# Optimization experiments

Hardware: AMD Instinct MI355X
Metric: run time of the kernel (lower is better)

The kernel has to match this reference:

```python
import jax, jax.numpy as jnp
import numpy as np

NUM_HEADS = 16
NEG_INF = -1e18


def setup_inputs() -> dict:
    key = jax.random.key(0)
    ks = jax.random.split(key, 9)
    T, B, D = 2048, 2, 1024
    s = 1.0 / np.sqrt(D)
    return {
        "query": jax.random.normal(ks[0], (T, B, D), jnp.float32),
        "q_w": jax.random.normal(ks[1], (D, D), jnp.float32) * s,
        "q_b": jax.random.normal(ks[2], (D,), jnp.float32) * 0.02,
        "k_w": jax.random.normal(ks[3], (D, D), jnp.float32) * s,
        "k_b": jax.random.normal(ks[4], (D,), jnp.float32) * 0.02,
        "v_w": jax.random.normal(ks[5], (D, D), jnp.float32) * s,
        "v_b": jax.random.normal(ks[6], (D,), jnp.float32) * 0.02,
        "out_w": jax.random.normal(ks[7], (D, D), jnp.float32) * s,
        "out_b": jax.random.normal(ks[8], (D,), jnp.float32) * 0.02,
    }


def reference(query, q_w, q_b, k_w, k_b, v_w, v_b, out_w, out_b):
    # query: [T, B, D] (Time x Batch x Channel). Self-attention, causal mask,
    # dropout=0, need_weights=True.
    T, B, D = query.shape
    H = NUM_HEADS
    hd = D // H
    scaling = 1.0 / jnp.sqrt(jnp.asarray(hd, query.dtype))

    q = (query @ q_w.T + q_b) * scaling
    k = query @ k_w.T + k_b
    v = query @ v_w.T + v_b

    def split_heads(x):  # [T, B, D] -> [B, H, T, hd]
        return x.reshape(T, B, H, hd).transpose(1, 2, 0, 3)

    qh, kh, vh = split_heads(q), split_heads(k), split_heads(v)

    # scores: [B, H, T, T]
    scores = jnp.einsum("bhtd,bhsd->bhts", qh, kh)
    causal = jnp.triu(jnp.full((T, T), NEG_INF, dtype=scores.dtype), k=1)
    scores = scores + causal

    probs = jax.nn.softmax(scores, axis=-1)
    attn = jnp.einsum("bhts,bhsd->bhtd", probs, vh)  # [B, H, T, hd]
    attn = attn.transpose(2, 0, 1, 3).reshape(T, B, D)
    out = attn @ out_w.T + out_b

    # averaged attention weights over heads: [B, T, T]
    avg_weights = probs.sum(axis=1) / H
    return out, avg_weights
```

## Files before the change

kernel.cpp:

```cpp
#include <hip/hip_runtime.h>
#include <hip/hip_bf16.h>
#include <stdint.h>

typedef __hip_bfloat16 bf16;
using short8 = __attribute__((ext_vector_type(8))) short;
using f32x4  = __attribute__((ext_vector_type(4))) float;

#define TDIM 2048
#define BDIM 2
#define DDIM 1024
#define HNUM 16
#define HD   64
#define MDIM 4096
#define M0   16.0f
#define L2E  1.44269504088896f
#define M0B  23.0831207f

__device__ __forceinline__ f32x4 mfma16(short8 a, short8 b, f32x4 c) {
  return __builtin_amdgcn_mfma_f32_16x16x32_bf16(a, b, c, 0, 0, 0);
}

__device__ __forceinline__ float fexp2(float s) {
  return __builtin_amdgcn_exp2f(__builtin_fmaf(s, L2E, -M0B));
}

union S8 { short8 v; bf16 h[8]; };
union P4 { uint2 u; bf16 h[4]; };

__global__ __launch_bounds__(256) void cast_all_kernel(
    const float* __restrict__ q, const float* __restrict__ wq,
    const float* __restrict__ wk, const float* __restrict__ wv,
    const float* __restrict__ wo, bf16* __restrict__ dst) {
  int t4 = blockIdx.x * blockDim.x + threadIdx.x;
  int idx = t4 * 4;
  const float* s;
  if (idx < 4194304)      s = q  + idx;
  else if (idx < 5242880) s = wq + (idx - 4194304);
  else if (idx < 6291456) s = wk + (idx - 5242880);
  else if (idx < 7340032) s = wv + (idx - 6291456);
  else                    s = wo + (idx - 7340032);
  float4 v = *(const float4*)s;
  union { ushort4 u; bf16 b[4]; } pk;
  pk.b[0] = __float2bfloat16(v.x);
  pk.b[1] = __float2bfloat16(v.y);
  pk.b[2] = __float2bfloat16(v.z);
  pk.b[3] = __float2bfloat16(v.w);
  *(ushort4*)(dst + idx) = pk.u;
}

__global__ __launch_bounds__(256, 2) void qkv_kernel(
    const bf16* __restrict__ X, const bf16* __restrict__ Wq,
    const bf16* __restrict__ Wk, const bf16* __restrict__ Wv,
    const float* __restrict__ qb, const float* __restrict__ kb,
    const float* __restrict__ vb, bf16* __restrict__ Qo,
    bf16* __restrict__ Ko, bf16* __restrict__ Vto) {
  __shared__ __align__(16) bf16 Xs[128][72];
  __shared__ __align__(16) bf16 Qs[64][72];
  __shared__ __align__(16) bf16 Ks[64][72];
  __shared__ __align__(16) bf16 Vs[64][72];
  const int tid  = threadIdx.x;
  const int lane = tid & 63, wave = tid >> 6;
  const int m0 = blockIdx.y * 128, n0 = blockIdx.x * 64;
  const int wm = (wave >> 1) * 64, wn = (wave & 1) * 32;
  const int fr = lane & 15, quad = lane >> 4, q8 = quad * 8;
  const int r = tid >> 3, cc = (tid & 7) * 8;
  f32x4 aq[4][2] = {}, ak[4][2] = {}, av[2][4] = {};
  const bf16* xp = X  + (size_t)(m0 + r) * DDIM + cc;
  const bf16* qp = Wq + (size_t)(n0 + r) * DDIM + cc;
  const bf16* kp = Wk + (size_t)(n0 + r) * DDIM + cc;
  const bf16* vp = Wv + (size_t)(n0 + r) * DDIM + cc;
  uint4 xv0, xv1, xv2, xv3, qv0, qv1, kv0, kv1, vv0, vv1;
#define QKV_LD(K0)                                                  \
  do {                                                              \
    xv0 = *(const uint4*)(xp + (K0));                               \
    xv1 = *(const uint4*)(xp + (size_t)32 * DDIM + (K0));           \
    xv2 = *(const uint4*)(xp + (size_t)64 * DDIM + (K0));           \
    xv3 = *(const uint4*)(xp + (size_t)96 * DDIM + (K0));           \
    qv0 = *(const uint4*)(qp + (K0));                               \
    qv1 = *(const uint4*)(qp + (size_t)32 * DDIM + (K0));           \
    kv0 = *(const uint4*)(kp + (K0));                               \
    kv1 = *(const uint4*)(kp + (size_t)32 * DDIM + (K0));           \
    vv0 = *(const uint4*)(vp + (K0));                               \
    vv1 = *(const uint4*)(vp + (size_t)32 * DDIM + (K0));           \
  } while (0)
  QKV_LD(0);
  for (int k0 = 0; k0 < DDIM; k0 += 64) {
    __syncthreads();
    *(uint4*)&Xs[r][cc]      = xv0;
    *(uint4*)&Xs[r + 32][cc] = xv1;
    *(uint4*)&Xs[r + 64][cc] = xv2;
    *(uint4*)&Xs[r + 96][cc] = xv3;
    *(uint4*)&Qs[r][cc]      = qv0;
    *(uint4*)&Qs[r + 32][cc] = qv1;
    *(uint4*)&Ks[r][cc]      = kv0;
    *(uint4*)&Ks[r + 32][cc] = kv1;
    *(uint4*)&Vs[r][cc]      = vv0;
    *(uint4*)&Vs[r + 32][cc] = vv1;
    __syncthreads();
    if (k0 + 64 < DDIM) QKV_LD(k0 + 64);
#pragma unroll
    for (int kk = 0; kk < 2; kk++) {
      const int ko = kk * 32 + q8;
      short8 xf[4], qf[2], kf[2], vf[2];
#pragma unroll
      for (int i = 0; i < 4; i++)
        xf[i] = *(const short8*)&Xs[wm + i * 16 + fr][ko];
#pragma unroll
      for (int j = 0; j < 2; j++) {
        qf[j] = *(const short8*)&Qs[wn + j * 16 + fr][ko];
        kf[j] = *(const short8*)&Ks[wn + j * 16 + fr][ko];
        vf[j] = *(const short8*)&Vs[wn + j * 16 + fr][ko];
      }
#pragma unroll
      for (int i = 0; i < 4; i++)
#pragma unroll
        for (int j = 0; j < 2; j++) {
          aq[i][j] = mfma16(xf[i], qf[j], aq[i][j]);
          ak[i][j] = mfma16(xf[i], kf[j], ak[i][j]);
          av[j][i] = mfma16(vf[j], xf[i], av[j][i]);
        }
    }
  }
#undef QKV_LD
#pragma unroll
  for (int mt = 0; mt < 4; mt++)
#pragma unroll
    for (int nt = 0; nt < 2; nt++)
#pragma unroll
      for (int i = 0; i < 4; i++) {
        int gm = m0 + wm + mt * 16 + quad * 4 + i;
        int gn = n0 + wn + nt * 16 + fr;
        int t = gm >> 1, bb = gm & 1, h = gn >> 6, e = gn & 63;
        size_t o = ((size_t)(bb * HNUM + h) * TDIM + t) * HD + e;
        Qo[o] = __float2bfloat16((aq[mt][nt][i] + qb[gn]) * 0.125f);
        Ko[o] = __float2bfloat16(ak[mt][nt][i] + kb[gn]);
      }
#pragma unroll
  for (int vt = 0; vt < 2; vt++)
#pragma unroll
    for (int xt = 0; xt < 4; xt++)
#pragma unroll
      for (int i = 0; i < 4; i++) {
        int gf = n0 + wn + vt * 16 + quad * 4 + i;
        int gt = m0 + wm + xt * 16 + fr;
        int t = gt >> 1, bb = gt & 1, h = gf >> 6, e = gf & 63;
        Vto[((size_t)(bb * HNUM + h) * HD + e) * TDIM + t] =
            __float2bfloat16(av[vt][xt][i] + vb[gf]);
      }
}

__global__ __launch_bounds__(256) void gemm_out_kernel(
    const bf16* __restrict__ P0, const bf16* __restrict__ P1,
    const bf16* __restrict__ Bw, const float* __restrict__ l0buf,
    const float* __restrict__ l1buf, const float* __restrict__ bias,
    float* __restrict__ of32) {
  __shared__ __align__(16) bf16 As[64][72];
  __shared__ __align__(16) bf16 Bs[64][72];
  __shared__ float sInv[64][16];
  const int tid  = threadIdx.x;
  const int lane = tid & 63, wave = tid >> 6;
  const int m0 = blockIdx.y * 64, n0 = blockIdx.x * 64;
  const int wm = (wave >> 1) * 32, wn = (wave & 1) * 32;
  const int fr = lane & 15, quad = lane >> 4, q8 = quad * 8;
  const int ldr = tid >> 3, ldc = (tid & 7) * 8;
#pragma unroll
  for (int e = 0; e < 4; e++) {
    int idx = tid * 4 + e;
    int row = idx >> 4, h = idx & 15;
    int gm = m0 + row, t = gm >> 1, bb = gm & 1;
    size_t li = (size_t)(bb * HNUM + h) * TDIM + t;
    sInv[row][h] = 1.0f / (l0buf[li] + l1buf[li]);
  }
  f32x4 acc[2][2] = {};
  const size_t ar0 = (size_t)(m0 + ldr) * DDIM + ldc;
  const size_t ar1 = ar0 + (size_t)32 * DDIM;
  const bf16* bp0 = Bw + (size_t)(n0 + ldr) * DDIM + ldc;
  const bf16* bp1 = bp0 + (size_t)32 * DDIM;
  short8 p00v, p10v, p01v, p11v;
  uint4 bv0, bv1;
#define OUT_LD(K0)                                  \
  do {                                              \
    p00v = *(const short8*)&P0[ar0 + (K0)];         \
    p10v = *(const short8*)&P1[ar0 + (K0)];         \
    p01v = *(const short8*)&P0[ar1 + (K0)];         \
    p11v = *(const short8*)&P1[ar1 + (K0)];         \
    bv0  = *(const uint4*)(bp0 + (K0));             \
    bv1  = *(const uint4*)(bp1 + (K0));             \
  } while (0)
  OUT_LD(0);
  __syncthreads();
  for (int k0 = 0; k0 < DDIM; k0 += 64) {
    const float inv0 = sInv[ldr][k0 >> 6];
    const float inv1 = sInv[ldr + 32][k0 >> 6];
    S8 s00, s10, s01, s11, w0, w1;
    s00.v = p00v; s10.v = p10v; s01.v = p01v; s11.v = p11v;
#pragma unroll
    for (int k = 0; k < 8; k++) {
      w0.h[k] = __float2bfloat16(
          (__bfloat162float(s00.h[k]) + __bfloat162float(s10.h[k])) * inv0);
      w1.h[k] = __float2bfloat16(
          (__bfloat162float(s01.h[k]) + __bfloat162float(s11.h[k])) * inv1);
    }
    __syncthreads();
    *(short8*)&As[ldr][ldc]      = w0.v;
    *(short8*)&As[ldr + 32][ldc] = w1.v;
    *(uint4*)&Bs[ldr][ldc]       = bv0;
    *(uint4*)&Bs[ldr + 32][ldc]  = bv1;
    __syncthreads();
    if (k0 + 64 < DDIM) OUT_LD(k0 + 64);
#pragma unroll
    for (int kk = 0; kk < 2; kk++) {
      const int ko = kk * 32 + q8;
      short8 af0, af1, bf0, bf1;
      af0 = *(const short8*)&As[wm + fr][ko];
      af1 = *(const short8*)&As[wm + 16 + fr][ko];
      bf0 = *(const short8*)&Bs[wn + fr][ko];
      bf1 = *(const short8*)&Bs[wn + 16 + fr][ko];
      acc[0][0] = mfma16(af0, bf0, acc[0][0]);
      acc[0][1] = mfma16(af0, bf1, acc[0][1]);
      acc[1][0] = mfma16(af1, bf0, acc[1][0]);
      acc[1][1] = mfma16(af1, bf1, acc[1][1]);
    }
  }
#undef OUT_LD
#pragma unroll
  for (int mt = 0; mt < 2; mt++)
#pragma unroll
    for (int nt = 0; nt < 2; nt++)
#pragma unroll
      for (int i = 0; i < 4; i++) {
        int gm = m0 + wm + mt * 16 + quad * 4 + i;
        int gn = n0 + wn + nt * 16 + fr;
        of32[(size_t)gm * DDIM + gn] = acc[mt][nt][i] + bias[gn];
      }
}

__global__ __launch_bounds__(256) void attn_split_kernel(
    const bf16* __restrict__ Q, const bf16* __restrict__ K,
    const bf16* __restrict__ Vt, bf16* __restrict__ P0o,
    bf16* __restrict__ P1o, float* __restrict__ l0buf,
    float* __restrict__ l1buf) {
  __shared__ __align__(16) bf16 Ks[2][64][40];
  __shared__ __align__(16) bf16 Vs[2][64][40];
  __shared__ __align__(16) bf16 pt[4][32][72];
  const int tid = threadIdx.x, lane = tid & 63, wave = tid >> 6;
  const int bid = blockIdx.x;
  const int part = bid & 1, bh = (bid >> 1) & 31, t128 = 15 - (bid >> 6);
  const int b = bh >> 4, h = bh & 15;
  const int t0 = t128 * 128 + wave * 32;
  const int fr = lane & 15, quad = lane >> 4, q8 = quad * 8;
  const bf16* Qp = Q + ((size_t)bh * TDIM + t0) * HD;
  const bf16* Kp = K + (size_t)bh * TDIM * HD;
  const bf16* Vp = Vt + (size_t)bh * HD * TDIM;
  short8 aq[2][2];
  aq[0][0] = *(const short8*)&Qp[fr * HD + q8];
  aq[0][1] = *(const short8*)&Qp[fr * HD + 32 + q8];
  aq[1][0] = *(const short8*)&Qp[(16 + fr) * HD + q8];
  aq[1][1] = *(const short8*)&Qp[(16 + fr) * HD + 32 + q8];
  const int Cb = 2 * t128 + 2, C0 = t128 + 1;
  const int clo = part ? C0 : 0, chi = part ? Cb : C0;
  const int sr0 = tid >> 3, scc = (tid & 7) * 8, sr1 = sr0 + 32;
  const int ssub = scc >> 5, scol = scc & 31;
  f32x4 oacc[2][4] = {};
  float lsum[2] = {0.f, 0.f};
  uint4 kv0, kv1, vv0, vv1;
  auto ldglob = [&](int c) {
    int s0 = c * 64;
    kv0 = *(const uint4*)&Kp[(size_t)(s0 + sr0) * HD + scc];
    kv1 = *(const uint4*)&Kp[(size_t)(s0 + sr1) * HD + scc];
    vv0 = *(const uint4*)&Vp[(size_t)sr0 * TDIM + s0 + scc];
    vv1 = *(const uint4*)&Vp[(size_t)sr1 * TDIM + s0 + scc];
  };
  ldglob(clo);
  for (int c = clo; c < chi; c++) {
    __syncthreads();
    *(uint4*)&Ks[ssub][sr0][scol] = kv0;
    *(uint4*)&Ks[ssub][sr1][scol] = kv1;
    *(uint4*)&Vs[ssub][sr0][scol] = vv0;
    *(uint4*)&Vs[ssub][sr1][scol] = vv1;
    __syncthreads();
    if (c + 1 < chi) ldglob(c + 1);
    const int s0 = c * 64;
    if (s0 > t0 + 31) continue;
    f32x4 scT[2][4] = {};
#pragma unroll
    for (int j = 0; j < 4; j++) {
      short8 k0f = *(const short8*)&Ks[0][j * 16 + fr][q8];
      short8 k1f = *(const short8*)&Ks[1][j * 16 + fr][q8];
      scT[0][j] = mfma16(k0f, aq[0][0], scT[0][j]);
      scT[0][j] = mfma16(k1f, aq[0][1], scT[0][j]);
      scT[1][j] = mfma16(k0f, aq[1][0], scT[1][j]);
      scT[1][j] = mfma16(k1f, aq[1][1], scT[1][j]);
    }
#pragma unroll
    for (int g = 0; g < 2; g++) {
      const int tg = t0 + g * 16;
#pragma unroll
      for (int j = 0; j < 4; j++) {
        const int sj = s0 + j * 16;
        P4 pk;
        if (sj > tg + 15) {
          pk.u = make_uint2(0u, 0u);
        } else if (sj + 15 <= tg) {
#pragma unroll
          for (int i = 0; i < 4; i++) {
            float p = fexp2(scT[g][j][i]);
            lsum[g] += p;
            pk.h[i] = __float2bfloat16(p);
          }
        } else {
          const int t_row = tg + fr;
          const int s_base = sj + quad * 4;
#pragma unroll
          for (int i = 0; i < 4; i++) {
            float p = 0.f;
            if (s_base + i <= t_row) {
              p = fexp2(scT[g][j][i]);
              lsum[g] += p;
            }
            pk.h[i] = __float2bfloat16(p);
          }
        }
        *(uint2*)&pt[wave][g * 16 + fr][j * 16 + quad * 4] = pk.u;
      }
    }
#pragma unroll
    for (int c2 = 0; c2 < 2; c2++) {
      short8 ap0 = *(const short8*)&pt[wave][fr][c2 * 32 + q8];
      short8 ap1 = *(const short8*)&pt[wave][16 + fr][c2 * 32 + q8];
#pragma unroll
      for (int nt = 0; nt < 4; nt++) {
        short8 vf = *(const short8*)&Vs[c2][nt * 16 + fr][q8];
        oacc[0][nt] = mfma16(ap0, vf, oacc[0][nt]);
        oacc[1][nt] = mfma16(ap1, vf, oacc[1][nt]);
      }
    }
  }
  float lr[2];
#pragma unroll
  for (int g = 0; g < 2; g++) {
    float l = lsum[g];
    l += __shfl_xor(l, 16);
    l += __shfl_xor(l, 32);
    lr[g] = l;
  }
  bf16*  Op = part ? P1o : P0o;
  float* lb = part ? l1buf : l0buf;
#pragma unroll
  for (int g = 0; g < 2; g++)
#pragma unroll
    for (int nt = 0; nt < 4; nt++)
#pragma unroll
      for (int i = 0; i < 4; i++) {
        int t_row = t0 + g * 16 + quad * 4 + i;
        int col = h * HD + nt * 16 + fr;
        Op[((size_t)t_row * BDIM + b) * DDIM + col] =
            __float2bfloat16(oacc[g][nt][i]);
      }
  if (quad == 0) {
    lb[(size_t)bh * TDIM + t0 + fr]      = lr[0];
    lb[(size_t)bh * TDIM + t0 + 16 + fr] = lr[1];
  }
}

__global__ __launch_bounds__(256) void avg_kernel(
    const bf16* __restrict__ Q, const bf16* __restrict__ K,
    const float* __restrict__ l0buf, const float* __restrict__ l1buf,
    float* __restrict__ avgw) {
  const int tid = threadIdx.x;
  int r = blockIdx.x;
  const int b = (r >= 1024) ? 1 : 0;
  r &= 1023;
  float* avp = avgw + (size_t)b * TDIM * TDIM;
  if (r >= 528) {
    int r2 = r - 528;
    int ti = 0;
    while (ti < 31 && 31 * (ti + 1) - (ti + 1) * ti / 2 <= r2) ti++;
    int si = ti + 1 + (r2 - (31 * ti - ti * (ti - 1) / 2));
    int t0b = ti * 64, s0 = si * 64;
#pragma unroll
    for (int k = 0; k < 4; k++) {
      int e = tid * 4 + k * 1024;
      *(float4*)&avp[(size_t)(t0b + (e >> 6)) * TDIM + s0 + (e & 63)] =
          make_float4(0.f, 0.f, 0.f, 0.f);
    }
    return;
  }
  int ti = 0;
  while ((ti + 1) * (ti + 2) / 2 <= r) ti++;
  const int si = r - ti * (ti + 1) / 2;
  const int t0b = ti * 64, s0 = si * 64;
  const bool isdiag = (si == ti);

  __shared__ __align__(16) bf16 Qs[2][2][64][40];
  __shared__ __align__(16) bf16 Ks2[2][2][64][40];
  __shared__ float sinvl[HNUM][64];
#pragma unroll
  for (int k = 0; k < 4; k++) {
    int idx = tid + k * 256;
    size_t li = (size_t)(b * HNUM + (idx >> 6)) * TDIM + t0b + (idx & 63);
    sinvl[idx >> 6][idx & 63] = 1.0f / (l0buf[li] + l1buf[li]);
  }
  const int lane = tid & 63, wave = tid >> 6;
  const int fr = lane & 15, quad = lane >> 4, q8 = quad * 8;
  const int twr = wave * 16;
  const int qr0 = tid >> 3, qcc = (tid & 7) * 8;
  const int qsub = qcc >> 5, qcol = qcc & 31;
  const bf16* Qb = Q + (size_t)b * HNUM * TDIM * HD;
  const bf16* Kb = K + (size_t)b * HNUM * TDIM * HD;
  uint4 qv0, qv1, kva, kvb;
#define AVG_LDH(HH)                                                     \
  do {                                                                  \
    const bf16* Qh = Qb + (size_t)(HH) * TDIM * HD;                     \
    const bf16* Kh = Kb + (size_t)(HH) * TDIM * HD;                     \
    qv0 = *(const uint4*)&Qh[(size_t)(t0b + qr0) * HD + qcc];           \
    qv1 = *(const uint4*)&Qh[(size_t)(t0b + qr0 + 32) * HD + qcc];      \
    kva = *(const uint4*)&Kh[(size_t)(s0 + qr0) * HD + qcc];            \
    kvb = *(const uint4*)&Kh[(size_t)(s0 + qr0 + 32) * HD + qcc];       \
  } while (0)
#define AVG_WR(B)                                                       \
  do {                                                                  \
    *(uint4*)&Qs[B][qsub][qr0][qcol]       = qv0;                       \
    *(uint4*)&Qs[B][qsub][qr0 + 32][qcol]  = qv1;                       \
    *(uint4*)&Ks2[B][qsub][qr0][qcol]      = kva;                       \
    *(uint4*)&Ks2[B][qsub][qr0 + 32][qcol] = kvb;                       \
  } while (0)
  AVG_LDH(0);
  AVG_WR(0);
  AVG_LDH(1);
  f32x4 facc[4] = {};
  const int ntlive = isdiag ? wave : 3;
  for (int hh = 0; hh < HNUM; hh++) {
    const int cur = hh & 1;
    __syncthreads();
    if (hh + 1 < HNUM) AVG_WR(cur ^ 1);
    if (hh + 2 < HNUM) AVG_LDH(hh + 2);
    short8 a0 = *(const short8*)&Qs[cur][0][twr + fr][q8];
    short8 a1 = *(const short8*)&Qs[cur][1][twr + fr][q8];
#pragma unroll
    for (int nt = 0; nt < 4; nt++) {
      if (nt > ntlive) continue;
      short8 b0 = *(const short8*)&Ks2[cur][0][nt * 16 + fr][q8];
      short8 b1 = *(const short8*)&Ks2[cur][1][nt * 16 + fr][q8];
      f32x4 sc = {};
      sc = mfma16(a0, b0, sc);
      sc = mfma16(a1, b1, sc);
      if (isdiag && nt == wave) {
#pragma unroll
        for (int i = 0; i < 4; i++) {
          if (fr <= quad * 4 + i)
            facc[nt][i] += fexp2(sc[i]) * sinvl[hh][twr + quad * 4 + i];
        }
      } else {
#pragma unroll
        for (int i = 0; i < 4; i++)
          facc[nt][i] += fexp2(sc[i]) * sinvl[hh][twr + quad * 4 + i];
      }
    }
  }
#undef AVG_LDH
#undef AVG_WR
#pragma unroll
  for (int nt = 0; nt < 4; nt++)
#pragma unroll
    for (int i = 0; i < 4; i++)
      avp[(size_t)(t0b + twr + quad * 4 + i) * TDIM + s0 + nt * 16 + fr] =
          facc[nt][i] * 0.0625f;
}

extern "C" void kernel_launch(void* const* d_in, const int* in_sizes, int n_in,
                              void* d_out, int out_size, void* d_ws, size_t ws_size,
                              hipStream_t stream) {
  const float* q   = (const float*)d_in[0];
  const float* q_w = (const float*)d_in[1];
  const float* q_b = (const float*)d_in[2];
  const float* k_w = (const float*)d_in[3];
  const float* k_b = (const float*)d_in[4];
  const float* v_w = (const float*)d_in[5];
  const float* v_b = (const float*)d_in[6];
  const float* o_w = (const float*)d_in[7];
  const float* o_b = (const float*)d_in[8];
  float* out = (float*)d_out;
  float* avg = out + (size_t)MDIM * DDIM;

  bf16* ws  = (bf16*)d_ws;
  bf16* Xbf = ws;
  bf16* Wq  = ws + 4194304;
  bf16* Wk  = ws + 5242880;
  bf16* Wv  = ws + 6291456;
  bf16* Wo  = ws + 7340032;
  bf16* Qw  = ws + 8388608;
  bf16* Kw  = ws + 12582912;
  bf16* Vt  = ws + 16777216;
  bf16* P1  = ws + 20971520;
  bf16* P0  = ws;
  float* l0 = (float*)(ws + 4194304);
  float* l1 = (float*)(ws + 4325376);

  cast_all_kernel<<<8192, 256, 0, stream>>>(q, q_w, k_w, v_w, o_w, Xbf);
  qkv_kernel<<<dim3(16, 32), 256, 0, stream>>>(Xbf, Wq, Wk, Wv, q_b, k_b, v_b,
                                               Qw, Kw, Vt);
  attn_split_kernel<<<1024, 256, 0, stream>>>(Qw, Kw, Vt, P0, P1, l0, l1);
  avg_kernel<<<2048, 256, 0, stream>>>(Qw, Kw, l0, l1, avg);
  gemm_out_kernel<<<dim3(16, 64), 256, 0, stream>>>(P0, P1, Wo, l0, l1, o_b, out);
}
```

Measured before the change: 237.8 us.

## Split split-attention combine into its own kernel and halve avg tile width

A separate combine kernel now sums the two partial attention outputs and normalises them once into a bf16 buffer, so the output GEMM loads a single A operand instead of two partials plus inverse-sum lookups per tile. The averaged-weights kernel now uses 64x32 tiles instead of 64x64 with twice as many blocks, and applies a per-16-column causal mask test so fully masked sub-tiles are skipped. This adds an extra launch and a round trip through memory for the combined buffer, and duplicates Q loads across the narrower avg tiles.

```diff
diff --git a/kernel.cpp b/kernel.cpp
--- a/kernel.cpp
+++ b/kernel.cpp
@@ -149,63 +149,56 @@
       }
 }
 
+__global__ __launch_bounds__(256) void combine_kernel(
+    const bf16* __restrict__ P0, const bf16* __restrict__ P1,
+    const float* __restrict__ l0buf, const float* __restrict__ l1buf,
+    bf16* __restrict__ A) {
+  const int idx = (blockIdx.x * 256 + threadIdx.x) * 8;
+  const int m = idx >> 10, col = idx & 1023;
+  const int t = m >> 1, bb = m & 1, h = col >> 6;
+  const size_t li = (size_t)(bb * HNUM + h) * TDIM + t;
+  const float inv = 1.0f / (l0buf[li] + l1buf[li]);
+  S8 a0, a1, w;
+  a0.v = *(const short8*)&P0[idx];
+  a1.v = *(const short8*)&P1[idx];
+#pragma unroll
+  for (int k = 0; k < 8; k++)
+    w.h[k] = __float2bfloat16(
+        (__bfloat162float(a0.h[k]) + __bfloat162float(a1.h[k])) * inv);
+  *(short8*)&A[idx] = w.v;
+}
+
 __global__ __launch_bounds__(256) void gemm_out_kernel(
-    const bf16* __restrict__ P0, const bf16* __restrict__ P1,
-    const bf16* __restrict__ Bw, const float* __restrict__ l0buf,
-    const float* __restrict__ l1buf, const float* __restrict__ bias,
-    float* __restrict__ of32) {
+    const bf16* __restrict__ A, const bf16* __restrict__ Bw,
+    const float* __restrict__ bias, float* __restrict__ of32) {
   __shared__ __align__(16) bf16 As[64][72];
   __shared__ __align__(16) bf16 Bs[64][72];
-  __shared__ float sInv[64][16];
   const int tid  = threadIdx.x;
   const int lane = tid & 63, wave = tid >> 6;
   const int m0 = blockIdx.y * 64, n0 = blockIdx.x * 64;
   const int wm = (wave >> 1) * 32, wn = (wave & 1) * 32;
   const int fr = lane & 15, quad = lane >> 4, q8 = quad * 8;
   const int ldr = tid >> 3, ldc = (tid & 7) * 8;
-#pragma unroll
-  for (int e = 0; e < 4; e++) {
-    int idx = tid * 4 + e;
-    int row = idx >> 4, h = idx & 15;
-    int gm = m0 + row, t = gm >> 1, bb = gm & 1;
-    size_t li = (size_t)(bb * HNUM + h) * TDIM + t;
-    sInv[row][h] = 1.0f / (l0buf[li] + l1buf[li]);
-  }
   f32x4 acc[2][2] = {};
-  const size_t ar0 = (size_t)(m0 + ldr) * DDIM + ldc;
-  const size_t ar1 = ar0 + (size_t)32 * DDIM;
+  const bf16* ap0 = A + (size_t)(m0 + ldr) * DDIM + ldc;
+  const bf16* ap1 = ap0 + (size_t)32 * DDIM;
   const bf16* bp0 = Bw + (size_t)(n0 + ldr) * DDIM + ldc;
   const bf16* bp1 = bp0 + (size_t)32 * DDIM;
-  short8 p00v, p10v, p01v, p11v;
-  uint4 bv0, bv1;
+  uint4 av0, av1, bv0, bv1;
 #define OUT_LD(K0)                                  \
   do {                                              \
-    p00v = *(const short8*)&P0[ar0 + (K0)];         \
-    p10v = *(const short8*)&P1[ar0 + (K0)];         \
-    p01v = *(const short8*)&P0[ar1 + (K0)];         \
-    p11v = *(const short8*)&P1[ar1 + (K0)];         \
-    bv0  = *(const uint4*)(bp0 + (K0));             \
-    bv1  = *(const uint4*)(bp1 + (K0));             \
+    av0 = *(const uint4*)(ap0 + (K0));              \
+    av1 = *(const uint4*)(ap1 + (K0));              \
+    bv0 = *(const uint4*)(bp0 + (K0));              \
+    bv1 = *(const uint4*)(bp1 + (K0));              \
   } while (0)
   OUT_LD(0);
-  __syncthreads();
   for (int k0 = 0; k0 < DDIM; k0 += 64) {
-    const float inv0 = sInv[ldr][k0 >> 6];
-    const float inv1 = sInv[ldr + 32][k0 >> 6];
-    S8 s00, s10, s01, s11, w0, w1;
-    s00.v = p00v; s10.v = p10v; s01.v = p01v; s11.v = p11v;
-#pragma unroll
-    for (int k = 0; k < 8; k++) {
-      w0.h[k] = __float2bfloat16(
-          (__bfloat162float(s00.h[k]) + __bfloat162float(s10.h[k])) * inv0);
-      w1.h[k] = __float2bfloat16(
-          (__bfloat162float(s01.h[k]) + __bfloat162float(s11.h[k])) * inv1);
-    }
-    __syncthreads();
-    *(short8*)&As[ldr][ldc]      = w0.v;
-    *(short8*)&As[ldr + 32][ldc] = w1.v;
-    *(uint4*)&Bs[ldr][ldc]       = bv0;
-    *(uint4*)&Bs[ldr + 32][ldc]  = bv1;
+    __syncthreads();
+    *(uint4*)&As[ldr][ldc]      = av0;
+    *(uint4*)&As[ldr + 32][ldc] = av1;
+    *(uint4*)&Bs[ldr][ldc]      = bv0;
+    *(uint4*)&Bs[ldr + 32][ldc] = bv1;
     __syncthreads();
     if (k0 + 64 < DDIM) OUT_LD(k0 + 64);
 #pragma unroll
@@ -369,31 +362,30 @@
     float* __restrict__ avgw) {
   const int tid = threadIdx.x;
   int r = blockIdx.x;
-  const int b = (r >= 1024) ? 1 : 0;
-  r &= 1023;
+  const int b = (r >= 2048) ? 1 : 0;
+  r &= 2047;
   float* avp = avgw + (size_t)b * TDIM * TDIM;
-  if (r >= 528) {
-    int r2 = r - 528;
+  if (r >= 1056) {
+    int r2 = r - 1056;
     int ti = 0;
-    while (ti < 31 && 31 * (ti + 1) - (ti + 1) * ti / 2 <= r2) ti++;
-    int si = ti + 1 + (r2 - (31 * ti - ti * (ti - 1) / 2));
-    int t0b = ti * 64, s0 = si * 64;
-#pragma unroll
-    for (int k = 0; k < 4; k++) {
-      int e = tid * 4 + k * 1024;
-      *(float4*)&avp[(size_t)(t0b + (e >> 6)) * TDIM + s0 + (e & 63)] =
+    while (ti < 31 && (ti + 1) * (62 - ti) <= r2) ti++;
+    int si = (2 * ti + 2) + (r2 - ti * (63 - ti));
+    int t0b = ti * 64, s0 = si * 32;
+#pragma unroll
+    for (int k = 0; k < 2; k++) {
+      int off = (tid * 2 + k) * 4;
+      *(float4*)&avp[(size_t)(t0b + (off >> 5)) * TDIM + s0 + (off & 31)] =
           make_float4(0.f, 0.f, 0.f, 0.f);
     }
     return;
   }
   int ti = 0;
-  while ((ti + 1) * (ti + 2) / 2 <= r) ti++;
-  const int si = r - ti * (ti + 1) / 2;
-  const int t0b = ti * 64, s0 = si * 64;
-  const bool isdiag = (si == ti);
+  while ((ti + 1) * (ti + 2) <= r) ti++;
+  const int si = r - ti * (ti + 1);
+  const int t0b = ti * 64, s0 = si * 32;
 
   __shared__ __align__(16) bf16 Qs[2][2][64][40];
-  __shared__ __align__(16) bf16 Ks2[2][2][64][40];
+  __shared__ __align__(16) bf16 Ks2[2][2][32][40];
   __shared__ float sinvl[HNUM][64];
 #pragma unroll
   for (int k = 0; k < 4; k++) {
@@ -403,65 +395,79 @@
   }
   const int lane = tid & 63, wave = tid >> 6;
   const int fr = lane & 15, quad = lane >> 4, q8 = quad * 8;
-  const int twr = wave * 16;
+  const int twr = wave * 16, tw = t0b + twr;
   const int qr0 = tid >> 3, qcc = (tid & 7) * 8;
   const int qsub = qcc >> 5, qcol = qcc & 31;
   const bf16* Qb = Q + (size_t)b * HNUM * TDIM * HD;
   const bf16* Kb = K + (size_t)b * HNUM * TDIM * HD;
-  uint4 qv0, qv1, kva, kvb;
+  uint4 qv0, qv1, kv1;
 #define AVG_LDH(HH)                                                     \
   do {                                                                  \
     const bf16* Qh = Qb + (size_t)(HH) * TDIM * HD;                     \
     const bf16* Kh = Kb + (size_t)(HH) * TDIM * HD;                     \
     qv0 = *(const uint4*)&Qh[(size_t)(t0b + qr0) * HD + qcc];           \
     qv1 = *(const uint4*)&Qh[(size_t)(t0b + qr0 + 32) * HD + qcc];      \
-    kva = *(const uint4*)&Kh[(size_t)(s0 + qr0) * HD + qcc];            \
-    kvb = *(const uint4*)&Kh[(size_t)(s0 + qr0 + 32) * HD + qcc];       \
+    kv1 = *(const uint4*)&Kh[(size_t)(s0 + qr0) * HD + qcc];            \
   } while (0)
 #define AVG_WR(B)                                                       \
   do {                                                                  \
-    *(uint4*)&Qs[B][qsub][qr0][qcol]       = qv0;                       \
-    *(uint4*)&Qs[B][qsub][qr0 + 32][qcol]  = qv1;                       \
-    *(uint4*)&Ks2[B][qsub][qr0][qcol]      = kva;                       \
-    *(uint4*)&Ks2[B][qsub][qr0 + 32][qcol] = kvb;                       \
+    *(uint4*)&Qs[B][qsub][qr0][qcol]      = qv0;                        \
+    *(uint4*)&Qs[B][qsub][qr0 + 32][qcol] = qv1;                        \
+    *(uint4*)&Ks2[B][qsub][qr0][qcol]     = kv1;                        \
   } while (0)
   AVG_LDH(0);
   AVG_WR(0);
   AVG_LDH(1);
-  f32x4 facc[4] = {};
-  const int ntlive = isdiag ? wave : 3;
+  f32x4 facc[2] = {};
+  const bool d0 = (s0 > tw + 15),      f0 = (s0 + 15 <= tw);
+  const bool d1 = (s0 + 16 > tw + 15), f1 = (s0 + 31 <= tw);
   for (int hh = 0; hh < HNUM; hh++) {
     const int cur = hh & 1;
     __syncthreads();
     if (hh + 1 < HNUM) AVG_WR(cur ^ 1);
     if (hh + 2 < HNUM) AVG_LDH(hh + 2);
+    f32x4 sv = *(const f32x4*)&sinvl[hh][twr + quad * 4];
     short8 a0 = *(const short8*)&Qs[cur][0][twr + fr][q8];
     short8 a1 = *(const short8*)&Qs[cur][1][twr + fr][q8];
-#pragma unroll
-    for (int nt = 0; nt < 4; nt++) {
-      if (nt > ntlive) continue;
-      short8 b0 = *(const short8*)&Ks2[cur][0][nt * 16 + fr][q8];
-      short8 b1 = *(const short8*)&Ks2[cur][1][nt * 16 + fr][q8];
+    if (!d0) {
+      short8 b0 = *(const short8*)&Ks2[cur][0][fr][q8];
+      short8 b1 = *(const short8*)&Ks2[cur][1][fr][q8];
       f32x4 sc = {};
       sc = mfma16(a0, b0, sc);
       sc = mfma16(a1, b1, sc);
-      if (isdiag && nt == wave) {
-#pragma unroll
-        for (int i = 0; i < 4; i++) {
-          if (fr <= quad * 4 + i)
-            facc[nt][i] += fexp2(sc[i]) * sinvl[hh][twr + quad * 4 + i];
-        }
+      if (f0) {
+#pragma unroll
+        for (int i = 0; i < 4; i++)
+          facc[0][i] += fexp2(sc[i]) * sv[i];
       } else {
 #pragma unroll
         for (int i = 0; i < 4; i++)
-          facc[nt][i] += fexp2(sc[i]) * sinvl[hh][twr + quad * 4 + i];
+          if (s0 + fr <= tw + quad * 4 + i)
+            facc[0][i] += fexp2(sc[i]) * sv[i];
+      }
+    }
+    if (!d1) {
+      short8 b0 = *(const short8*)&Ks2[cur][0][16 + fr][q8];
+      short8 b1 = *(const short8*)&Ks2[cur][1][16 + fr][q8];
+      f32x4 sc = {};
+      sc = mfma16(a0, b0, sc);
+      sc = mfma16(a1, b1, sc);
+      if (f1) {
+#pragma unroll
+        for (int i = 0; i < 4; i++)
+          facc[1][i] += fexp2(sc[i]) * sv[i];
+      } else {
+#pragma unroll
+        for (int i = 0; i < 4; i++)
+          if (s0 + 16 + fr <= tw + quad * 4 + i)
+            facc[1][i] += fexp2(sc[i]) * sv[i];
       }
     }
   }
 #undef AVG_LDH
 #undef AVG_WR
 #pragma unroll
-  for (int nt = 0; nt < 4; nt++)
+  for (int nt = 0; nt < 2; nt++)
 #pragma unroll
     for (int i = 0; i < 4; i++)
       avp[(size_t)(t0b + twr + quad * 4 + i) * TDIM + s0 + nt * 16 + fr] =
@@ -494,6 +500,7 @@
   bf16* Vt  = ws + 16777216;
   bf16* P1  = ws + 20971520;
   bf16* P0  = ws;
+  bf16* Ab  = ws + 16777216;
   float* l0 = (float*)(ws + 4194304);
   float* l1 = (float*)(ws + 4325376);
 
@@ -501,6 +508,7 @@
   qkv_kernel<<<dim3(16, 32), 256, 0, stream>>>(Xbf, Wq, Wk, Wv, q_b, k_b, v_b,
                                                Qw, Kw, Vt);
   attn_split_kernel<<<1024, 256, 0, stream>>>(Qw, Kw, Vt, P0, P1, l0, l1);
-  avg_kernel<<<2048, 256, 0, stream>>>(Qw, Kw, l0, l1, avg);
-  gemm_out_kernel<<<dim3(16, 64), 256, 0, stream>>>(P0, P1, Wo, l0, l1, o_b, out);
-}
+  combine_kernel<<<2048, 256, 0, stream>>>(P0, P1, l0, l1, Ab);
+  avg_kernel<<<4096, 256, 0, stream>>>(Qw, Kw, l0, l1, avg);
+  gemm_out_kernel<<<dim3(16, 64), 256, 0, stream>>>(Ab, Wo, o_b, out);
+}
```

Result: faster. 223.5 us (-6.0%).
